# Kernel optimization log

Measured on AMD Instinct MI355X. Metric: run time of the kernel, lower is better.

The kernel has to match this reference:

```python
import jax, jax.numpy as jnp
import numpy as np
from jax.scipy.special import erfc

CUTOFF = 10.0   # real-space cutoff (Angstrom)
ALPHA = 0.3     # Ewald splitting parameter (1/Angstrom)
KMAX = 8        # max integer k-index per dimension
N_ATOMS = 4096
BOX = 40.0      # cubic box edge (Angstrom)


def setup_inputs() -> dict:
    key = jax.random.key(0)
    kp, kq = jax.random.split(key)
    positions = jax.random.uniform(kp, (N_ATOMS, 3), dtype=jnp.float32) * BOX
    charges = jax.random.normal(kq, (N_ATOMS,), dtype=jnp.float32)
    charges = charges - charges.mean()  # enforce charge neutrality
    cell = jnp.eye(3, dtype=jnp.float32) * BOX  # row-vector lattice
    return {"positions": positions, "charges": charges, "cell": cell}


def _kvectors(kmax):
    # static integer grid (-kmax..kmax)^3 \\ {0}, built with numpy at trace time
    n = np.arange(-kmax, kmax + 1)
    grid = np.stack(np.meshgrid(n, n, n, indexing="ij"), axis=-1).reshape(-1, 3)
    grid = grid[np.any(grid != 0, axis=-1)]
    return jnp.asarray(grid, dtype=jnp.float32)  # [Nk, 3]


def _ewald(positions, charges, cell, cutoff, alpha, kmax):
    N = positions.shape[0]
    inv_cell = jnp.linalg.inv(cell)

    # ---- real-space sum: 0.5 * sum_{i!=j, r<rc} q_i q_j erfc(a r)/r (min image)
    rij = positions[:, None, :] - positions[None, :, :]          # [N,N,3]
    frac = rij @ inv_cell
    rij = (frac - jnp.round(frac)) @ cell                        # minimum image
    r2 = jnp.sum(rij * rij, axis=-1)                             # [N,N]
    eye = jnp.eye(N, dtype=bool)
    r = jnp.sqrt(jnp.where(eye, 1.0, r2))                        # safe sqrt on diag
    pair_mask = (~eye) & (r2 < cutoff * cutoff)
    qq = charges[:, None] * charges[None, :]
    e_real = 0.5 * jnp.sum(jnp.where(pair_mask, qq * erfc(alpha * r) / r, 0.0))

    # ---- reciprocal-space sum: (2pi/V) sum_k exp(-k^2/4a^2)/k^2 |S(k)|^2
    recip = 2.0 * jnp.pi * inv_cell.T                            # reciprocal lattice rows
    kvecs = _kvectors(kmax) @ recip                              # [Nk,3]
    k2 = jnp.sum(kvecs * kvecs, axis=-1)                         # [Nk]
    phase = positions @ kvecs.T                                  # [N,Nk]
    s_re = charges @ jnp.cos(phase)                              # [Nk]
    s_im = charges @ jnp.sin(phase)                              # [Nk]
    vol = jnp.abs(jnp.linalg.det(cell))
    coeff = jnp.exp(-k2 / (4.0 * alpha * alpha)) / k2
    e_recip = (2.0 * jnp.pi / vol) * jnp.sum(coeff * (s_re * s_re + s_im * s_im))

    # ---- self-energy correction
    e_self = -(alpha / jnp.sqrt(jnp.pi)) * jnp.sum(charges * charges)

    return e_real + e_recip + e_self


def reference(positions, charges, cell):
    return _ewald(positions, charges, cell, CUTOFF, ALPHA, KMAX)
```

## Files before the change

kernel.cpp:

```cpp
#include <hip/hip_runtime.h>
#include <math.h>

#define ALPHA 0.3f
#define KMAX 8
#define KDIM 17
#define KD2 (KDIM*KDIM)
#define NK_FULL (KDIM*KDIM*KDIM - 1)
#define NK_HALF (NK_FULL/2)
#define RECIP_KPB 16
#define NB_RECIP ((NK_HALF + RECIP_KPB - 1)/RECIP_KPB)
#define TWO_PI 6.28318530717958647692f

#define SELF_COEF (-0.16925687506432687f)
#define INV_4A2 (1.0f/(4.0f*ALPHA*ALPHA))
#define C1A (0.3275911f*ALPHA)
#define NA2 (-(ALPHA*ALPHA))

#define ITILE 256
#define JTILE 128

__device__ __forceinline__ void invert3x3(const float* __restrict__ c, float inv[9], float* det_out) {
    float a00=c[0],a01=c[1],a02=c[2];
    float a10=c[3],a11=c[4],a12=c[5];
    float a20=c[6],a21=c[7],a22=c[8];
    float c00 =  a11*a22 - a12*a21;
    float c01 = -(a10*a22 - a12*a20);
    float c02 =  a10*a21 - a11*a20;
    float det = a00*c00 + a01*c01 + a02*c02;
    float id = 1.0f/det;
    inv[0] =  c00*id;
    inv[1] = -(a01*a22 - a02*a21)*id;
    inv[2] =  (a01*a12 - a02*a11)*id;
    inv[3] =  c01*id;
    inv[4] =  (a00*a22 - a02*a20)*id;
    inv[5] = -(a00*a12 - a02*a10)*id;
    inv[6] =  c02*id;
    inv[7] = -(a00*a21 - a01*a20)*id;
    inv[8] =  (a00*a11 - a01*a10)*id;
    *det_out = det;
}

__device__ __forceinline__ float erfc_a(float r, float r2) {
    float t = __builtin_amdgcn_rcpf(fmaf(C1A, r, 1.0f));
    float p = t * fmaf(t, fmaf(t, fmaf(t, fmaf(t, 1.061405429f, -1.453152027f),
                       1.421413741f), -0.284496736f), 0.254829592f);
    return p * __expf(NA2 * r2);
}

__device__ __forceinline__ float pair_ortho(float4 p, float xi, float yi, float zi,
                                            float i0, float i4, float i8,
                                            float c0, float c4, float c8) {
    float dx = xi - p.x, dy = yi - p.y, dz = zi - p.z;
    float rx = fmaf(-c0, rintf(dx * i0), dx);
    float ry = fmaf(-c4, rintf(dy * i4), dy);
    float rz = fmaf(-c8, rintf(dz * i8), dz);
    float r2 = fmaf(rx, rx, fmaf(ry, ry, rz * rz));
    float rinv = __builtin_amdgcn_rsqf(r2);
    float r = r2 * rinv;
    return p.w * rinv * erfc_a(r, r2);
}

__device__ __forceinline__ float block_reduce(float v) {
    for (int o = 32; o > 0; o >>= 1) v += __shfl_down(v, o, 64);
    __shared__ float smem[4];
    int lane = threadIdx.x & 63, wid = threadIdx.x >> 6;
    if (lane == 0) smem[wid] = v;
    __syncthreads();
    int nw = blockDim.x >> 6;
    v = ((int)threadIdx.x < nw) ? smem[threadIdx.x] : 0.0f;
    if (wid == 0) {
        for (int o = 4; o > 0; o >>= 1) v += __shfl_down(v, o, 64);
    }
    return v;
}

__global__ __launch_bounds__(256) void fused_kernel(const float* __restrict__ pos,
                                                    const float* __restrict__ q,
                                                    const float* __restrict__ cell,
                                                    float* __restrict__ e_out,
                                                    int N, int nb_recip, int nb_real) {
    __shared__ float4 tile2[2][256];
    __shared__ float red_re[4][RECIP_KPB];
    __shared__ float red_im[4][RECIP_KPB];
    float inv[9]; float det;
    invert3x3(cell, inv, &det);
    bool ortho = (cell[1]==0.f) & (cell[2]==0.f) & (cell[3]==0.f) &
                 (cell[5]==0.f) & (cell[6]==0.f) & (cell[7]==0.f);

    int bid = blockIdx.x;
    int tid = threadIdx.x;
    int lane = tid & 63, wid = tid >> 6;

    if (bid < nb_recip) {
        int kbase = bid * RECIP_KPB;
        int kslot = tid & 15;
        int agrp  = tid >> 4;
        int kk = kbase + kslot;
        int kc = (kk < NK_HALF) ? kk : 0;
        float kx = (float)(kc / KD2 - KMAX);
        float ky = (float)((kc / KDIM) % KDIM - KMAX);
        float kz = (float)(kc % KDIM - KMAX);

        int nrounds = (N + 255) >> 8;

        if (tid < N) {
            int a = tid;
            float x = pos[3*a], y = pos[3*a+1], z = pos[3*a+2];
            float wx, wy, wz;
            if (ortho) { wx = x*inv[0]; wy = y*inv[4]; wz = z*inv[8]; }
            else {
                wx = inv[0]*x + inv[3]*y + inv[6]*z;
                wy = inv[1]*x + inv[4]*y + inv[7]*z;
                wz = inv[2]*x + inv[5]*y + inv[8]*z;
            }
            tile2[0][tid] = make_float4(wx, wy, wz, q[a]);
        }
        __syncthreads();

        float sre0 = 0.0f, sim0 = 0.0f, sre1 = 0.0f, sim1 = 0.0f;
        for (int r = 0; r < nrounds; ++r) {
            int base = r << 8;
            int cnt = min(256, N - base);
            int abase = base + 256;
            bool pf = (abase + tid) < N;
            float4 nxt = make_float4(0.f, 0.f, 0.f, 0.f);
            if (pf) {
                int a = abase + tid;
                float x = pos[3*a], y = pos[3*a+1], z = pos[3*a+2];
                float wx, wy, wz;
                if (ortho) { wx = x*inv[0]; wy = y*inv[4]; wz = z*inv[8]; }
                else {
                    wx = inv[0]*x + inv[3]*y + inv[6]*z;
                    wy = inv[1]*x + inv[4]*y + inv[7]*z;
                    wz = inv[2]*x + inv[5]*y + inv[8]*z;
                }
                nxt = make_float4(wx, wy, wz, q[a]);
            }
            const float4* buf = tile2[r & 1];
            int s0 = agrp * 16;
            int s1 = min(s0 + 16, cnt);
            int t = s0;
            #pragma unroll 4
            for (; t + 1 < s1; t += 2) {
                float4 w0 = buf[t], w1 = buf[t + 1];
                float ph0 = fmaf(kx, w0.x, fmaf(ky, w0.y, kz * w0.z));
                float ph1 = fmaf(kx, w1.x, fmaf(ky, w1.y, kz * w1.z));
                ph0 -= rintf(ph0);
                ph1 -= rintf(ph1);
                sre0 = fmaf(w0.w, __builtin_amdgcn_cosf(ph0), sre0);
                sim0 = fmaf(w0.w, __builtin_amdgcn_sinf(ph0), sim0);
                sre1 = fmaf(w1.w, __builtin_amdgcn_cosf(ph1), sre1);
                sim1 = fmaf(w1.w, __builtin_amdgcn_sinf(ph1), sim1);
            }
            for (; t < s1; ++t) {
                float4 w = buf[t];
                float ph = fmaf(kx, w.x, fmaf(ky, w.y, kz * w.z));
                ph -= rintf(ph);
                sre0 = fmaf(w.w, __builtin_amdgcn_cosf(ph), sre0);
                sim0 = fmaf(w.w, __builtin_amdgcn_sinf(ph), sim0);
            }
            if (pf) tile2[(r + 1) & 1][tid] = nxt;
            __syncthreads();
        }
        float sre = sre0 + sre1, sim = sim0 + sim1;

        sre += __shfl_xor(sre, 16, 64);  sim += __shfl_xor(sim, 16, 64);
        sre += __shfl_xor(sre, 32, 64);  sim += __shfl_xor(sim, 32, 64);
        if (lane < RECIP_KPB) { red_re[wid][kslot] = sre; red_im[wid][kslot] = sim; }
        __syncthreads();
        if (wid == 0) {
            float e = 0.0f;
            if (lane < RECIP_KPB) {
                float sr = red_re[0][lane] + red_re[1][lane] + red_re[2][lane] + red_re[3][lane];
                float si = red_im[0][lane] + red_im[1][lane] + red_im[2][lane] + red_im[3][lane];
                int t = kbase + lane;
                if (t < NK_HALF) {
                    float nx = (float)(t / KD2 - KMAX);
                    float ny = (float)((t / KDIM) % KDIM - KMAX);
                    float nz = (float)(t % KDIM - KMAX);
                    float kvx = TWO_PI * (nx*inv[0] + ny*inv[1] + nz*inv[2]);
                    float kvy = TWO_PI * (nx*inv[3] + ny*inv[4] + nz*inv[5]);
                    float kvz = TWO_PI * (nx*inv[6] + ny*inv[7] + nz*inv[8]);
                    float k2 = fmaf(kvx, kvx, fmaf(kvy, kvy, kvz * kvz));
                    float vol = fabsf(det);
                    float pref = 2.0f * (TWO_PI / vol);
                    float coeff = __expf(-k2 * INV_4A2) * __builtin_amdgcn_rcpf(k2);
                    e = pref * coeff * fmaf(sr, sr, si * si);
                }
            }
            for (int o = 8; o > 0; o >>= 1) e += __shfl_down(e, o, 64);
            if (lane == 0) unsafeAtomicAdd(e_out, e);
        }
        if (bid == nb_recip - 1) {
            float fa = 0.0f;
            for (int t = tid; t < N; t += 256) {
                float qt = q[t];
                fa = fmaf(SELF_COEF * qt, qt, fa);
            }
            __syncthreads();
            float s2 = block_reduce(fa);
            if (tid == 0) unsafeAtomicAdd(e_out, s2);
        }
    } else {
        int rbid = bid - nb_recip;
        int bi = 0, acc = 0;
        for (;;) {
            int up = min(N, (bi + 1) * ITILE);
            int nc = (up + JTILE - 1) / JTILE;
            if (rbid < acc + nc) break;
            acc += nc; ++bi;
        }
        int bj = rbid - acc;

        float c0 = cell[0], c4 = cell[4], c8 = cell[8];
        float c1 = cell[1], c2 = cell[2], c3 = cell[3];
        float c5 = cell[5], c6 = cell[6], c7 = cell[7];

        int ibase = bi * ITILE;
        int i = ibase + tid;
        bool ivalid = (i < N);
        float xi = 0.f, yi = 0.f, zi = 0.f, qi = 0.f;
        if (ivalid) { xi = pos[3*i]; yi = pos[3*i+1]; zi = pos[3*i+2]; qi = q[i]; }

        int jbase = bj * JTILE;
        int jcount = min(JTILE, N - jbase);
        float4* tile = tile2[0];
        if (tid < jcount) {
            int j = jbase + tid;
            tile[tid] = make_float4(pos[3*j], pos[3*j+1], pos[3*j+2], q[j]);
        }
        __syncthreads();

        bool full = (jbase + JTILE <= ibase) && (ibase + ITILE <= N) && (jcount == JTILE);

        float e0 = 0.0f, e1 = 0.0f, e2 = 0.0f, e3 = 0.0f;
        if (ortho) {
            float i0 = inv[0], i4 = inv[4], i8 = inv[8];
            if (full) {
                #pragma unroll 2
                for (int t = 0; t < JTILE; t += 4) {
                    float4 p0 = tile[t+0], p1 = tile[t+1], p2 = tile[t+2], p3 = tile[t+3];
                    e0 += pair_ortho(p0, xi, yi, zi, i0, i4, i8, c0, c4, c8);
                    e1 += pair_ortho(p1, xi, yi, zi, i0, i4, i8, c0, c4, c8);
                    e2 += pair_ortho(p2, xi, yi, zi, i0, i4, i8, c0, c4, c8);
                    e3 += pair_ortho(p3, xi, yi, zi, i0, i4, i8, c0, c4, c8);
                }
            } else {
                int t = 0;
                for (; t + 3 < jcount; t += 4) {
                    float4 p0 = tile[t+0], p1 = tile[t+1], p2 = tile[t+2], p3 = tile[t+3];
                    float v0 = pair_ortho(p0, xi, yi, zi, i0, i4, i8, c0, c4, c8);
                    float v1 = pair_ortho(p1, xi, yi, zi, i0, i4, i8, c0, c4, c8);
                    float v2 = pair_ortho(p2, xi, yi, zi, i0, i4, i8, c0, c4, c8);
                    float v3 = pair_ortho(p3, xi, yi, zi, i0, i4, i8, c0, c4, c8);
                    bool k0 = ivalid && ((jbase + t + 0) < i);
                    bool k1 = ivalid && ((jbase + t + 1) < i);
                    bool k2 = ivalid && ((jbase + t + 2) < i);
                    bool k3 = ivalid && ((jbase + t + 3) < i);
                    e0 += k0 ? v0 : 0.0f;
                    e1 += k1 ? v1 : 0.0f;
                    e2 += k2 ? v2 : 0.0f;
                    e3 += k3 ? v3 : 0.0f;
                }
                for (; t < jcount; ++t) {
                    float4 p = tile[t];
                    float v = pair_ortho(p, xi, yi, zi, i0, i4, i8, c0, c4, c8);
                    bool ok = ivalid && ((jbase + t) < i);
                    e0 += ok ? v : 0.0f;
                }
            }
        } else {
            for (int t = 0; t < jcount; ++t) {
                float4 p = tile[t];
                float dx = xi - p.x, dy = yi - p.y, dz = zi - p.z;
                float fx = dx*inv[0] + dy*inv[3] + dz*inv[6];
                float fy = dx*inv[1] + dy*inv[4] + dz*inv[7];
                float fz = dx*inv[2] + dy*inv[5] + dz*inv[8];
                fx -= rintf(fx); fy -= rintf(fy); fz -= rintf(fz);
                float rx = fx*c0 + fy*c3 + fz*c6;
                float ry = fx*c1 + fy*c4 + fz*c7;
                float rz = fx*c2 + fy*c5 + fz*c8;
                float r2 = fmaf(rx, rx, fmaf(ry, ry, rz * rz));
                float rinv = __builtin_amdgcn_rsqf(r2);
                float r = r2 * rinv;
                float val = p.w * rinv * erfc_a(r, r2);
                bool ok = ivalid && ((jbase + t) < i);
                e0 += ok ? val : 0.0f;
            }
        }
        float acc_e = ((e0 + e1) + (e2 + e3)) * qi;

        float s = block_reduce(acc_e);
        if (tid == 0) unsafeAtomicAdd(e_out, s);
    }
}

extern "C" void kernel_launch(void* const* d_in, const int* in_sizes, int n_in,
                              void* d_out, int out_size, void* d_ws, size_t ws_size,
                              hipStream_t stream) {
    const float* pos  = (const float*)d_in[0];
    const float* q    = (const float*)d_in[1];
    const float* cell = (const float*)d_in[2];
    int N = in_sizes[1];
    float* e_out = (float*)d_out;

    int nbi = (N + ITILE - 1) / ITILE;
    int nb_real = 0;
    for (int bi = 0; bi < nbi; ++bi) {
        int up = (N < (bi + 1) * ITILE) ? N : (bi + 1) * ITILE;
        nb_real += (up + JTILE - 1) / JTILE;
    }
    int nb_recip = NB_RECIP;

    hipMemsetAsync(e_out, 0, sizeof(float), stream);

    fused_kernel<<<nb_recip + nb_real, 256, 0, stream>>>(pos, q, cell, e_out,
                                                         N, nb_recip, nb_real);
}
```

Measured before the change: 78.16 us.

## Compute recip structure factors via complex rotation recurrence per atom

Reciprocal blocks now map each thread to one atom instead of one k-vector. Each thread evaluates sin/cos only three times per atom: the base phase, the kz step, and a wrap step. It then walks all 16 consecutive k-vectors of the block by complex multiplication, keeping the 16 complex accumulators in registers. This replaces 16 sin/cos transcendental pairs per atom-k with cheap FMAs and removes the double-buffered LDS atom tile. The cost is a larger per-thread register footprint, a bigger LDS transpose reduction, and possible accumulated rounding error along the recurrence chain.

Result: faster. 73.65 us (-5.8%).

```diff
diff --git a/kernel.cpp b/kernel.cpp
--- a/kernel.cpp
+++ b/kernel.cpp
@@ -79,9 +79,9 @@
                                                     const float* __restrict__ cell,
                                                     float* __restrict__ e_out,
                                                     int N, int nb_recip, int nb_real) {
-    __shared__ float4 tile2[2][256];
-    __shared__ float red_re[4][RECIP_KPB];
-    __shared__ float red_im[4][RECIP_KPB];
+    __shared__ float4 rtile[256];
+    __shared__ float red[128][33];
+    __shared__ float red2[8][33];
     float inv[9]; float det;
     invert3x3(cell, inv, &det);
     bool ortho = (cell[1]==0.f) & (cell[2]==0.f) & (cell[3]==0.f) &
@@ -93,40 +93,25 @@
 
     if (bid < nb_recip) {
         int kbase = bid * RECIP_KPB;
-        int kslot = tid & 15;
-        int agrp  = tid >> 4;
-        int kk = kbase + kslot;
-        int kc = (kk < NK_HALF) ? kk : 0;
-        float kx = (float)(kc / KD2 - KMAX);
-        float ky = (float)((kc / KDIM) % KDIM - KMAX);
-        float kz = (float)(kc % KDIM - KMAX);
+        int m = kbase % KDIM;
+        int wj = (16 - m) % KDIM;
+        bool kxw = ((kbase + wj) % KD2) == (KD2 - 1);
+        int wj_s  = __builtin_amdgcn_readfirstlane(wj);
+        int kxw_s = __builtin_amdgcn_readfirstlane((int)kxw);
+        float fkx0 = (float)(kbase / KD2 - KMAX);
+        float fky0 = (float)((kbase / KDIM) % KDIM - KMAX);
+        float fkz0 = (float)(kbase % KDIM - KMAX);
+
+        float ar[RECIP_KPB], ai[RECIP_KPB];
+        #pragma unroll
+        for (int j = 0; j < RECIP_KPB; ++j) { ar[j] = 0.0f; ai[j] = 0.0f; }
 
         int nrounds = (N + 255) >> 8;
-
-        if (tid < N) {
-            int a = tid;
-            float x = pos[3*a], y = pos[3*a+1], z = pos[3*a+2];
-            float wx, wy, wz;
-            if (ortho) { wx = x*inv[0]; wy = y*inv[4]; wz = z*inv[8]; }
-            else {
-                wx = inv[0]*x + inv[3]*y + inv[6]*z;
-                wy = inv[1]*x + inv[4]*y + inv[7]*z;
-                wz = inv[2]*x + inv[5]*y + inv[8]*z;
-            }
-            tile2[0][tid] = make_float4(wx, wy, wz, q[a]);
-        }
-        __syncthreads();
-
-        float sre0 = 0.0f, sim0 = 0.0f, sre1 = 0.0f, sim1 = 0.0f;
         for (int r = 0; r < nrounds; ++r) {
-            int base = r << 8;
-            int cnt = min(256, N - base);
-            int abase = base + 256;
-            bool pf = (abase + tid) < N;
-            float4 nxt = make_float4(0.f, 0.f, 0.f, 0.f);
-            if (pf) {
-                int a = abase + tid;
+            int a = (r << 8) + tid;
+            if (a < N) {
                 float x = pos[3*a], y = pos[3*a+1], z = pos[3*a+2];
+                float qa = q[a];
                 float wx, wy, wz;
                 if (ortho) { wx = x*inv[0]; wy = y*inv[4]; wz = z*inv[8]; }
                 else {
@@ -134,46 +119,64 @@
                     wy = inv[1]*x + inv[4]*y + inv[7]*z;
                     wz = inv[2]*x + inv[5]*y + inv[8]*z;
                 }
-                nxt = make_float4(wx, wy, wz, q[a]);
-            }
-            const float4* buf = tile2[r & 1];
-            int s0 = agrp * 16;
-            int s1 = min(s0 + 16, cnt);
-            int t = s0;
+                float ph0 = fmaf(fkx0, wx, fmaf(fky0, wy, fkz0 * wz));
+                ph0 -= rintf(ph0);
+                float az = wz - rintf(wz);
+                float aw = kxw_s ? (wx - 16.0f*wy - 17.0f*wz)
+                                 : (wy - 17.0f*wz);
+                aw -= rintf(aw);
+                float c0 = __builtin_amdgcn_cosf(ph0), s0 = __builtin_amdgcn_sinf(ph0);
+                float zc = __builtin_amdgcn_cosf(az),  zs = __builtin_amdgcn_sinf(az);
+                float wc = __builtin_amdgcn_cosf(aw),  ws = __builtin_amdgcn_sinf(aw);
+                float pr = qa * c0, pi = qa * s0;
+                #pragma unroll
+                for (int j = 0; j < RECIP_KPB; ++j) {
+                    ar[j] += pr; ai[j] += pi;
+                    if (j < RECIP_KPB - 1) {
+                        float nr = pr*zc - pi*zs;
+                        float ni = pr*zs + pi*zc;
+                        pr = nr; pi = ni;
+                        if (j == wj_s) {
+                            nr = pr*wc - pi*ws;
+                            ni = pr*ws + pi*wc;
+                            pr = nr; pi = ni;
+                        }
+                    }
+                }
+            }
+        }
+
+        #pragma unroll
+        for (int j = 0; j < RECIP_KPB; ++j) {
+            ar[j] += __shfl_down(ar[j], 32, 64);
+            ai[j] += __shfl_down(ai[j], 32, 64);
+        }
+        if (lane < 32) {
+            int row = (wid << 5) | lane;
+            #pragma unroll
+            for (int j = 0; j < RECIP_KPB; ++j) {
+                red[row][j]             = ar[j];
+                red[row][RECIP_KPB + j] = ai[j];
+            }
+        }
+        __syncthreads();
+        {
+            int v = tid & 31, grp = tid >> 5;
+            float s = 0.0f;
+            int r0 = grp << 4;
             #pragma unroll 4
-            for (; t + 1 < s1; t += 2) {
-                float4 w0 = buf[t], w1 = buf[t + 1];
-                float ph0 = fmaf(kx, w0.x, fmaf(ky, w0.y, kz * w0.z));
-                float ph1 = fmaf(kx, w1.x, fmaf(ky, w1.y, kz * w1.z));
-                ph0 -= rintf(ph0);
-                ph1 -= rintf(ph1);
-                sre0 = fmaf(w0.w, __builtin_amdgcn_cosf(ph0), sre0);
-                sim0 = fmaf(w0.w, __builtin_amdgcn_sinf(ph0), sim0);
-                sre1 = fmaf(w1.w, __builtin_amdgcn_cosf(ph1), sre1);
-                sim1 = fmaf(w1.w, __builtin_amdgcn_sinf(ph1), sim1);
-            }
-            for (; t < s1; ++t) {
-                float4 w = buf[t];
-                float ph = fmaf(kx, w.x, fmaf(ky, w.y, kz * w.z));
-                ph -= rintf(ph);
-                sre0 = fmaf(w.w, __builtin_amdgcn_cosf(ph), sre0);
-                sim0 = fmaf(w.w, __builtin_amdgcn_sinf(ph), sim0);
-            }
-            if (pf) tile2[(r + 1) & 1][tid] = nxt;
-            __syncthreads();
-        }
-        float sre = sre0 + sre1, sim = sim0 + sim1;
-
-        sre += __shfl_xor(sre, 16, 64);  sim += __shfl_xor(sim, 16, 64);
-        sre += __shfl_xor(sre, 32, 64);  sim += __shfl_xor(sim, 32, 64);
-        if (lane < RECIP_KPB) { red_re[wid][kslot] = sre; red_im[wid][kslot] = sim; }
+            for (int rr = 0; rr < 16; ++rr) s += red[r0 + rr][v];
+            red2[grp][v] = s;
+        }
         __syncthreads();
-        if (wid == 0) {
+        if (tid < 32) {
+            float tot = 0.0f;
+            #pragma unroll
+            for (int g = 0; g < 8; ++g) tot += red2[g][tid];
+            float other = __shfl_down(tot, 16, 64);
             float e = 0.0f;
-            if (lane < RECIP_KPB) {
-                float sr = red_re[0][lane] + red_re[1][lane] + red_re[2][lane] + red_re[3][lane];
-                float si = red_im[0][lane] + red_im[1][lane] + red_im[2][lane] + red_im[3][lane];
-                int t = kbase + lane;
+            if (tid < 16) {
+                int t = kbase + tid;
                 if (t < NK_HALF) {
                     float nx = (float)(t / KD2 - KMAX);
                     float ny = (float)((t / KDIM) % KDIM - KMAX);
@@ -185,11 +188,11 @@
                     float vol = fabsf(det);
                     float pref = 2.0f * (TWO_PI / vol);
                     float coeff = __expf(-k2 * INV_4A2) * __builtin_amdgcn_rcpf(k2);
-                    e = pref * coeff * fmaf(sr, sr, si * si);
-                }
-            }
-            for (int o = 8; o > 0; o >>= 1) e += __shfl_down(e, o, 64);
-            if (lane == 0) unsafeAtomicAdd(e_out, e);
+                    e = pref * coeff * fmaf(tot, tot, other * other);
+                }
+                for (int o = 8; o > 0; o >>= 1) e += __shfl_down(e, o, 64);
+                if (tid == 0) unsafeAtomicAdd(e_out, e);
+            }
         }
         if (bid == nb_recip - 1) {
             float fa = 0.0f;
@@ -224,10 +227,9 @@
 
         int jbase = bj * JTILE;
         int jcount = min(JTILE, N - jbase);
-        float4* tile = tile2[0];
         if (tid < jcount) {
             int j = jbase + tid;
-            tile[tid] = make_float4(pos[3*j], pos[3*j+1], pos[3*j+2], q[j]);
+            rtile[tid] = make_float4(pos[3*j], pos[3*j+1], pos[3*j+2], q[j]);
         }
         __syncthreads();
 
@@ -239,7 +241,7 @@
             if (full) {
                 #pragma unroll 2
                 for (int t = 0; t < JTILE; t += 4) {
-                    float4 p0 = tile[t+0], p1 = tile[t+1], p2 = tile[t+2], p3 = tile[t+3];
+                    float4 p0 = rtile[t+0], p1 = rtile[t+1], p2 = rtile[t+2], p3 = rtile[t+3];
                     e0 += pair_ortho(p0, xi, yi, zi, i0, i4, i8, c0, c4, c8);
                     e1 += pair_ortho(p1, xi, yi, zi, i0, i4, i8, c0, c4, c8);
                     e2 += pair_ortho(p2, xi, yi, zi, i0, i4, i8, c0, c4, c8);
@@ -248,7 +250,7 @@
             } else {
                 int t = 0;
                 for (; t + 3 < jcount; t += 4) {
-                    float4 p0 = tile[t+0], p1 = tile[t+1], p2 = tile[t+2], p3 = tile[t+3];
+                    float4 p0 = rtile[t+0], p1 = rtile[t+1], p2 = rtile[t+2], p3 = rtile[t+3];
                     float v0 = pair_ortho(p0, xi, yi, zi, i0, i4, i8, c0, c4, c8);
                     float v1 = pair_ortho(p1, xi, yi, zi, i0, i4, i8, c0, c4, c8);
                     float v2 = pair_ortho(p2, xi, yi, zi, i0, i4, i8, c0, c4, c8);
@@ -263,7 +265,7 @@
                     e3 += k3 ? v3 : 0.0f;
                 }
                 for (; t < jcount; ++t) {
-                    float4 p = tile[t];
+                    float4 p = rtile[t];
                     float v = pair_ortho(p, xi, yi, zi, i0, i4, i8, c0, c4, c8);
                     bool ok = ivalid && ((jbase + t) < i);
                     e0 += ok ? v : 0.0f;
@@ -271,7 +273,7 @@
             }
         } else {
             for (int t = 0; t < jcount; ++t) {
-                float4 p = tile[t];
+                float4 p = rtile[t];
                 float dx = xi - p.x, dy = yi - p.y, dz = zi - p.z;
                 float fx = dx*inv[0] + dy*inv[3] + dz*inv[6];
                 float fy = dx*inv[1] + dy*inv[4] + dz*inv[7];
```
